# Kernel tuning notes

Measured on AMD Instinct MI355X. Metric: run time of the kernel, lower is better.

Reference implementation:

```python
import jax, jax.numpy as jnp
import numpy as np
import math

EMB_S = 64
HEADS = 8
EMB = EMB_S * HEADS  # 512
M = int(EMB_S * 0.5)  # 32 random features
B, T = 8, 4096
EPS = 1e-5


def setup_inputs() -> dict:
    key = jax.random.key(0)
    ks = jax.random.split(key, 16)
    s_in = 1.0 / math.sqrt(EMB_S)
    s_emb = 1.0 / math.sqrt(EMB)
    s_hid = 1.0 / math.sqrt(4 * EMB)
    return {
        "x": jax.random.normal(ks[0], (B, T, EMB), jnp.float32),
        "w": jax.random.normal(ks[1], (M, EMB_S), jnp.float32),  # frozen random features
        "kqv_w": jax.random.uniform(ks[2], (3 * EMB_S, EMB_S), jnp.float32, -s_in, s_in),
        "kqv_b": jax.random.uniform(ks[3], (3 * EMB_S,), jnp.float32, -s_in, s_in),
        "proj_w": jax.random.uniform(ks[4], (EMB, EMB), jnp.float32, -s_emb, s_emb),
        "proj_b": jax.random.uniform(ks[5], (EMB,), jnp.float32, -s_emb, s_emb),
        "ln1_g": 1.0 + 0.02 * jax.random.normal(ks[6], (EMB,), jnp.float32),
        "ln1_b": 0.02 * jax.random.normal(ks[7], (EMB,), jnp.float32),
        "ln2_g": 1.0 + 0.02 * jax.random.normal(ks[8], (EMB,), jnp.float32),
        "ln2_b": 0.02 * jax.random.normal(ks[9], (EMB,), jnp.float32),
        "mlp_w1": jax.random.uniform(ks[10], (4 * EMB, EMB), jnp.float32, -s_emb, s_emb),
        "mlp_b1": jax.random.uniform(ks[11], (4 * EMB,), jnp.float32, -s_emb, s_emb),
        "mlp_w2": jax.random.uniform(ks[12], (EMB, 4 * EMB), jnp.float32, -s_hid, s_hid),
        "mlp_b2": jax.random.uniform(ks[13], (EMB,), jnp.float32, -s_hid, s_hid),
    }


def _layer_norm(x, g, b):
    mu = jnp.mean(x, axis=-1, keepdims=True)
    var = jnp.mean(jnp.square(x - mu), axis=-1, keepdims=True)
    return (x - mu) * jax.lax.rsqrt(var + EPS) * g + b


def _prm_exp(z, w):
    # z: [B,T,H,E]; softmax-kernel random features, [B,T,H,M]
    xd = 0.5 * jnp.sum(z * z, axis=-1, keepdims=True)
    wtx = jnp.einsum("bthe,me->bthm", z, w)
    return jnp.exp(wtx - xd) / math.sqrt(M)


def reference(x, w, kqv_w, kqv_b, proj_w, proj_b, ln1_g, ln1_b, ln2_g, ln2_b,
              mlp_w1, mlp_b1, mlp_w2, mlp_b2):
    Bb, Tt, _ = x.shape
    h = _layer_norm(x, ln1_g, ln1_b).reshape(Bb, Tt, HEADS, EMB_S)
    kqv = jnp.einsum("bthe,fe->bthf", h, kqv_w) + kqv_b  # [B,T,H,3E]
    k, q, v = jnp.split(kqv, 3, axis=-1)  # torch.split order: k, q, v
    kp = _prm_exp(k, w)  # [B,T,H,M]
    qp = _prm_exp(q, w)
    D = jnp.einsum("bthm,bhm->bth", qp, kp.sum(axis=1))  # [B,T,H]
    kptv = jnp.einsum("bthe,bthm->bhem", v, kp)  # [B,H,E,M]
    y = jnp.einsum("bthm,bhem->bthe", qp, kptv) / D[..., None]
    y = y.reshape(Bb, Tt, EMB)
    attn = jnp.einsum("btf,ef->bte", y, proj_w) + proj_b  # dropout = identity (eval)
    x = x + attn
    h2 = _layer_norm(x, ln2_g, ln2_b)
    hid = jax.nn.gelu(jnp.einsum("bte,fe->btf", h2, mlp_w1) + mlp_b1, approximate=False)
    mlp_out = jnp.einsum("btf,ef->bte", hid, mlp_w2) + mlp_b2
    return x + mlp_out
```

## Files before the change

kernel.cpp:

```cpp
#include <hip/hip_runtime.h>
#include <hip/hip_bf16.h>

typedef __bf16 bf16x8_t __attribute__((ext_vector_type(8)));
typedef float f32x4_t __attribute__((ext_vector_type(4)));
using bf16 = __hip_bfloat16;

#define EMB 512
#define NTOK 32768
#define NROW 262144
#define SQRT_M_INV 0.17677669529663687f

__device__ __forceinline__ void gload16(const void* g, void* l) {
  __builtin_amdgcn_global_load_lds((const __attribute__((address_space(1))) void*)g,
                                   (__attribute__((address_space(3))) void*)l, 16, 0, 0);
}

__device__ __forceinline__ float fast_gelu(float v) {
  float u = v * 0.70710678118654752f;
  float a = fabsf(u);
  float tt = __builtin_amdgcn_rcpf(fmaf(0.3275911f, a, 1.0f));
  float p = fmaf(tt, 1.061405429f, -1.453152027f);
  p = fmaf(tt, p, 1.421413741f);
  p = fmaf(tt, p, -0.284496736f);
  p = fmaf(tt, p, 0.254829592f);
  p = p * tt;
  float e = __expf(-a * a);
  float er = fmaf(-p, e, 1.0f);
  er = copysignf(er, u);
  return 0.5f * v * (1.0f + er);
}

__device__ __forceinline__ void cvt4(const float* __restrict__ in,
                                     bf16* __restrict__ out, int i4, int n4) {
  if (i4 < n4) {
    float4 v = ((const float4*)in)[i4];
    alignas(8) bf16 o[4];
    o[0] = __float2bfloat16(v.x); o[1] = __float2bfloat16(v.y);
    o[2] = __float2bfloat16(v.z); o[3] = __float2bfloat16(v.w);
    *(uint2*)(out + i4 * 4) = *(const uint2*)o;
  }
}
__global__ __launch_bounds__(256) void f2b4_kernel(
    const float* __restrict__ a, bf16* __restrict__ oa, int na4,
    const float* __restrict__ b, bf16* __restrict__ ob, int nb4,
    const float* __restrict__ c, bf16* __restrict__ oc, int nc4,
    const float* __restrict__ d, bf16* __restrict__ od, int nd4) {
  int i4 = blockIdx.x * 256 + threadIdx.x;
  cvt4(a, oa, i4, na4);
  cvt4(b, ob, i4, nb4);
  cvt4(c, oc, i4, nc4);
  cvt4(d, od, i4, nd4);
}

__global__ __launch_bounds__(256) void ln_kernel(const float* __restrict__ x,
                                                 const float* __restrict__ g,
                                                 const float* __restrict__ bt,
                                                 bf16* __restrict__ out) {
  int lane = threadIdx.x & 63;
  int row = blockIdx.x * 4 + (threadIdx.x >> 6);
  const float* xr = x + (size_t)row * EMB;
  float4 v0 = ((const float4*)xr)[lane * 2];
  float4 v1 = ((const float4*)xr)[lane * 2 + 1];
  float s = v0.x + v0.y + v0.z + v0.w + v1.x + v1.y + v1.z + v1.w;
#pragma unroll
  for (int o = 32; o; o >>= 1) s += __shfl_xor(s, o);
  float mu = s * (1.0f / 512.0f);
  float vs = 0.f, d;
  d = v0.x - mu; vs += d * d;  d = v0.y - mu; vs += d * d;
  d = v0.z - mu; vs += d * d;  d = v0.w - mu; vs += d * d;
  d = v1.x - mu; vs += d * d;  d = v1.y - mu; vs += d * d;
  d = v1.z - mu; vs += d * d;  d = v1.w - mu; vs += d * d;
#pragma unroll
  for (int o = 32; o; o >>= 1) vs += __shfl_xor(vs, o);
  float rstd = rsqrtf(vs * (1.0f / 512.0f) + 1e-5f);
  float4 g0 = ((const float4*)g)[lane * 2], g1 = ((const float4*)g)[lane * 2 + 1];
  float4 b0 = ((const float4*)bt)[lane * 2], b1 = ((const float4*)bt)[lane * 2 + 1];
  alignas(16) bf16 o8[8];
  o8[0] = __float2bfloat16((v0.x - mu) * rstd * g0.x + b0.x);
  o8[1] = __float2bfloat16((v0.y - mu) * rstd * g0.y + b0.y);
  o8[2] = __float2bfloat16((v0.z - mu) * rstd * g0.z + b0.z);
  o8[3] = __float2bfloat16((v0.w - mu) * rstd * g0.w + b0.w);
  o8[4] = __float2bfloat16((v1.x - mu) * rstd * g1.x + b1.x);
  o8[5] = __float2bfloat16((v1.y - mu) * rstd * g1.y + b1.y);
  o8[6] = __float2bfloat16((v1.z - mu) * rstd * g1.z + b1.z);
  o8[7] = __float2bfloat16((v1.w - mu) * rstd * g1.w + b1.w);
  *(uint4*)(out + (size_t)row * EMB + lane * 8) = *(const uint4*)o8;
}

template <int BM, int BN, int WM, int WN, int OP>
__global__ __launch_bounds__(256) void gemm_bt(const bf16* __restrict__ A,
                                               const bf16* __restrict__ W,
                                               const float* __restrict__ bias,
                                               const float* __restrict__ res,
                                               float* __restrict__ outF,
                                               bf16* __restrict__ outB,
                                               int M, int N, int K) {
  constexpr int BK = 32;
  constexpr int TM = BM / WM, TN = BN / WN;
  constexpr int NI = TM / 16, NJ = TN / 16;
  constexpr int AP = BM * BK / 2048;
  constexpr int WP = BN * BK / 2048;
  alignas(16) __shared__ bf16 As[2][BM * BK];
  alignas(16) __shared__ bf16 Ws[2][BN * BK];
  int t = threadIdx.x;
  int lane = t & 63, wid = t >> 6;
  int wm = wid % WM, wn = wid / WM;
  int bn = blockIdx.x * BN, bm = blockIdx.y * BM;
  int lr = lane & 15, lq = lane >> 4;
  const int r0 = (t * 8) >> 5, c0 = (t * 8) & 31;

  const bf16* ap = A + (size_t)(bm + r0) * K + c0;
  const bf16* wp = W + (size_t)(bn + r0) * K + c0;
  const size_t strA = (size_t)64 * K;

  f32x4_t acc[NI][NJ];
#pragma unroll
  for (int i = 0; i < NI; ++i)
#pragma unroll
    for (int j = 0; j < NJ; ++j)
#pragma unroll
      for (int r = 0; r < 4; ++r) acc[i][j][r] = 0.f;

  auto stage = [&](int buf) {
#pragma unroll
    for (int p = 0; p < AP; ++p)
      gload16(ap + (size_t)p * strA, &As[buf][(r0 + p * 64) * BK + c0]);
#pragma unroll
    for (int p = 0; p < WP; ++p)
      gload16(wp + (size_t)p * strA, &Ws[buf][(r0 + p * 64) * BK + c0]);
    ap += BK;
    wp += BK;
  };
  auto compute = [&](int buf) {
    bf16x8_t afr[NI], bfr[NJ];
#pragma unroll
    for (int i = 0; i < NI; ++i)
      afr[i] = *(const bf16x8_t*)&As[buf][(wm * TM + i * 16 + lr) * BK + lq * 8];
#pragma unroll
    for (int j = 0; j < NJ; ++j)
      bfr[j] = *(const bf16x8_t*)&Ws[buf][(wn * TN + j * 16 + lr) * BK + lq * 8];
#pragma unroll
    for (int i = 0; i < NI; ++i)
#pragma unroll
      for (int j = 0; j < NJ; ++j)
        acc[i][j] = __builtin_amdgcn_mfma_f32_16x16x32_bf16(afr[i], bfr[j], acc[i][j], 0, 0, 0);
  };

  const int nt = K / BK;
  stage(0);
  int cur = 0;
  for (int kt = 0; kt < nt - 1; ++kt) {
    __syncthreads();
    stage(cur ^ 1);
    compute(cur);
    cur ^= 1;
  }
  __syncthreads();
  compute(cur);

#pragma unroll
  for (int i = 0; i < NI; ++i)
#pragma unroll
    for (int j = 0; j < NJ; ++j) {
      int gn = bn + wn * TN + j * 16 + lr;
      float bv = bias[gn];
#pragma unroll
      for (int r = 0; r < 4; ++r) {
        int gm = bm + wm * TM + i * 16 + lq * 4 + r;
        float v = acc[i][j][r] + bv;
        size_t off = (size_t)gm * N + gn;
        if (OP == 0) {
          outF[off] = v;
        } else if (OP == 1) {
          outF[off] = v + res[off];
        } else {
          outB[off] = __float2bfloat16(fast_gelu(v));
        }
      }
    }
}

__device__ __forceinline__ size_t bh_row(size_t grow) {
  size_t h = grow & 7, bt = grow >> 3;
  size_t b = bt >> 12, tt = bt & 4095;
  return ((b * 8 + h) << 12) + tt;
}

__global__ __launch_bounds__(256) void kqv_prm_kernel(
    const bf16* __restrict__ A,
    const bf16* __restrict__ Wk,
    const float* __restrict__ bias,
    const float* __restrict__ wrf,
    float* __restrict__ kp, float* __restrict__ qp,
    bf16* __restrict__ vout) {
  constexpr int LDZ = 136;
  constexpr int LDV = 72;
  alignas(16) __shared__ char u_raw[27648];
  bf16* As  = (bf16*)u_raw;
  bf16* Ws  = (bf16*)(u_raw + 4096);
  bf16* zkq = (bf16*)u_raw;
  bf16* vs  = (bf16*)(u_raw + 17408);
  float* xd_s = (float*)(u_raw + 26624);

  int t = threadIdx.x;
  int lane = t & 63, wid = t >> 6;
  int wm = wid & 1, wn = wid >> 1;
  int lr = lane & 15, lq = lane >> 4;
  size_t row0 = (size_t)blockIdx.x * 64;

  bf16x8_t wfrag[2][2];
#pragma unroll
  for (int mt = 0; mt < 2; ++mt)
#pragma unroll
    for (int ks = 0; ks < 2; ++ks) {
      const float* src = wrf + (mt * 16 + lr) * 64 + ks * 32 + lq * 8;
#pragma unroll
      for (int jj = 0; jj < 8; ++jj) wfrag[mt][ks][jj] = (__bf16)src[jj];
    }

  f32x4_t acc[2][6];
#pragma unroll
  for (int i = 0; i < 2; ++i)
#pragma unroll
    for (int j = 0; j < 6; ++j)
#pragma unroll
      for (int r = 0; r < 4; ++r) acc[i][j][r] = 0.f;

  const int r0 = t >> 2, c0 = (t * 8) & 31;
  for (int k0 = 0; k0 < 64; k0 += 32) {
    gload16(&A[(row0 + r0) * 64 + k0 + c0], &As[r0 * 32 + c0]);
#pragma unroll
    for (int p = 0; p < 3; ++p) {
      int r = r0 + p * 64;
      gload16(&Wk[(size_t)r * 64 + k0 + c0], &Ws[r * 32 + c0]);
    }
    __syncthreads();
    bf16x8_t af[2], bfr[6];
#pragma unroll
    for (int i = 0; i < 2; ++i)
      af[i] = *(const bf16x8_t*)&As[(wm * 32 + i * 16 + lr) * 32 + lq * 8];
#pragma unroll
    for (int j = 0; j < 6; ++j)
      bfr[j] = *(const bf16x8_t*)&Ws[(wn * 96 + j * 16 + lr) * 32 + lq * 8];
#pragma unroll
    for (int i = 0; i < 2; ++i)
#pragma unroll
      for (int j = 0; j < 6; ++j)
        acc[i][j] = __builtin_amdgcn_mfma_f32_16x16x32_bf16(af[i], bfr[j], acc[i][j], 0, 0, 0);
    __syncthreads();
  }

#pragma unroll
  for (int i = 0; i < 2; ++i)
#pragma unroll
    for (int j = 0; j < 6; ++j) {
      int col = wn * 96 + j * 16 + lr;
      float bv = bias[col];
      int rowb = wm * 32 + i * 16 + lq * 4;
#pragma unroll
      for (int r = 0; r < 4; ++r) {
        float v = acc[i][j][r] + bv;
        if (col < 128) zkq[(rowb + r) * LDZ + col] = __float2bfloat16(v);
        else           vs[(rowb + r) * LDV + (col - 128)] = __float2bfloat16(v);
      }
    }
  __syncthreads();

  if (t < 128) {
    int r = t & 63, sel = t >> 6;
    const bf16* zr = &zkq[r * LDZ + sel * 64];
    float xd = 0.f;
#pragma unroll
    for (int c = 0; c < 64; c += 8) {
      bf16x8_t z8 = *(const bf16x8_t*)&zr[c];
#pragma unroll
      for (int jj = 0; jj < 8; ++jj) { float f = (float)z8[jj]; xd += f * f; }
    }
    xd_s[r * 2 + sel] = 0.5f * xd;
  }
  __syncthreads();

#pragma unroll
  for (int p = 0; p < 2; ++p) {
    int idx = t + p * 256;
    int r = idx >> 3, c8 = idx & 7;
    size_t nr = bh_row(row0 + r);
    *(uint4*)&vout[nr * 64 + c8 * 8] = *(const uint4*)&vs[r * LDV + c8 * 8];
  }

  int sel = wn;
  f32x4_t aw[2][2];
#pragma unroll
  for (int i = 0; i < 2; ++i)
#pragma unroll
    for (int mt = 0; mt < 2; ++mt)
#pragma unroll
      for (int r = 0; r < 4; ++r) aw[i][mt][r] = 0.f;
#pragma unroll
  for (int ks = 0; ks < 2; ++ks) {
    bf16x8_t af2[2];
#pragma unroll
    for (int i = 0; i < 2; ++i)
      af2[i] = *(const bf16x8_t*)&zkq[(wm * 32 + i * 16 + lr) * LDZ + sel * 64 + ks * 32 + lq * 8];
#pragma unroll
    for (int i = 0; i < 2; ++i)
#pragma unroll
      for (int mt = 0; mt < 2; ++mt)
        aw[i][mt] = __builtin_amdgcn_mfma_f32_16x16x32_bf16(af2[i], wfrag[mt][ks], aw[i][mt], 0, 0, 0);
  }
  float* outp = sel ? qp : kp;
#pragma unroll
  for (int i = 0; i < 2; ++i)
#pragma unroll
    for (int r = 0; r < 4; ++r) {
      int row = wm * 32 + i * 16 + lq * 4 + r;
      size_t nr = bh_row(row0 + row);
#pragma unroll
      for (int mt = 0; mt < 2; ++mt) {
        int m = mt * 16 + lr;
        outp[nr * 32 + m] =
            __expf(aw[i][mt][r] - xd_s[row * 2 + sel]) * SQRT_M_INV;
      }
    }
}

__global__ __launch_bounds__(256) void kptv_kernel(const bf16* __restrict__ v2,
                                                   const float* __restrict__ kp2,
                                                   float* __restrict__ part) {
  int bh = blockIdx.x, chunk = blockIdx.y;
  int t = threadIdx.x, e = t & 63, g = t >> 6;
  const bf16* vp = v2 + ((size_t)bh * 4096 + chunk * 512) * 64 + e;
  const float* kpp = kp2 + ((size_t)bh * 4096 + chunk * 512) * 32 + g * 8;
  float acc[8] = {0.f, 0.f, 0.f, 0.f, 0.f, 0.f, 0.f, 0.f};
  float accs[8] = {0.f, 0.f, 0.f, 0.f, 0.f, 0.f, 0.f, 0.f};
#pragma unroll 8
  for (int tok = 0; tok < 512; ++tok) {
    float vv = __bfloat162float(vp[tok * 64]);
    float4 k0 = *(const float4*)(kpp + tok * 32);
    float4 k1 = *(const float4*)(kpp + tok * 32 + 4);
    acc[0] += vv * k0.x; acc[1] += vv * k0.y; acc[2] += vv * k0.z; acc[3] += vv * k0.w;
    acc[4] += vv * k1.x; acc[5] += vv * k1.y; acc[6] += vv * k1.z; acc[7] += vv * k1.w;
    accs[0] += k0.x; accs[1] += k0.y; accs[2] += k0.z; accs[3] += k0.w;
    accs[4] += k1.x; accs[5] += k1.y; accs[6] += k1.z; accs[7] += k1.w;
  }
  float* pp = part + (size_t)(bh * 8 + chunk) * 2080 + e * 32 + g * 8;
  *(float4*)pp = make_float4(acc[0], acc[1], acc[2], acc[3]);
  *(float4*)(pp + 4) = make_float4(acc[4], acc[5], acc[6], acc[7]);
  if (e == 0) {
    float* ps = part + (size_t)(bh * 8 + chunk) * 2080 + 2048 + g * 8;
    *(float4*)ps = make_float4(accs[0], accs[1], accs[2], accs[3]);
    *(float4*)(ps + 4) = make_float4(accs[4], accs[5], accs[6], accs[7]);
  }
}

__global__ __launch_bounds__(256) void y_kernel(const float* __restrict__ qp2,
                                                const float* __restrict__ part,
                                                bf16* __restrict__ y) {
  int bh = blockIdx.x, chunk = blockIdx.y;
  int b = bh >> 3, h = bh & 7;
  alignas(16) __shared__ float qp_s[16][32];
  int t = threadIdx.x;
  int e = t & 63, iq = t >> 6;
  float kv[32], ks[32];
#pragma unroll
  for (int m = 0; m < 32; ++m) { kv[m] = 0.f; ks[m] = 0.f; }
  for (int c = 0; c < 8; ++c) {
    const float* pp = part + (size_t)(bh * 8 + c) * 2080;
#pragma unroll
    for (int m = 0; m < 32; m += 4) {
      float4 a = *(const float4*)&pp[e * 32 + m];
      kv[m] += a.x; kv[m + 1] += a.y; kv[m + 2] += a.z; kv[m + 3] += a.w;
      float4 s = *(const float4*)&pp[2048 + m];
      ks[m] += s.x; ks[m + 1] += s.y; ks[m + 2] += s.z; ks[m + 3] += s.w;
    }
  }
  for (int grp = 0; grp < 32; ++grp) {
    int tok0 = chunk * 512 + grp * 16;
    __syncthreads();
    if (t < 128) {
      int r = t >> 3, c4 = t & 7;
      *(float4*)&qp_s[r][c4 * 4] =
          *(const float4*)(qp2 + ((size_t)bh * 4096 + tok0 + r) * 32 + c4 * 4);
    }
    __syncthreads();
#pragma unroll
    for (int i0 = 0; i0 < 4; ++i0) {
      int i = iq * 4 + i0;
      float dot = 0.f, dd = 0.f;
#pragma unroll
      for (int m = 0; m < 32; m += 4) {
        float4 qq = *(const float4*)&qp_s[i][m];
        dot += qq.x * kv[m] + qq.y * kv[m + 1] + qq.z * kv[m + 2] + qq.w * kv[m + 3];
        dd  += qq.x * ks[m] + qq.y * ks[m + 1] + qq.z * ks[m + 2] + qq.w * ks[m + 3];
      }
      y[(size_t)(b * 4096 + tok0 + i) * EMB + h * 64 + e] = __float2bfloat16(dot / dd);
    }
  }
}

extern "C" void kernel_launch(void* const* d_in, const int* in_sizes, int n_in,
                              void* d_out, int out_size, void* d_ws, size_t ws_size,
                              hipStream_t stream) {
  const float* x      = (const float*)d_in[0];
  const float* w      = (const float*)d_in[1];
  const float* kqv_w  = (const float*)d_in[2];
  const float* kqv_b  = (const float*)d_in[3];
  const float* proj_w = (const float*)d_in[4];
  const float* proj_b = (const float*)d_in[5];
  const float* ln1_g  = (const float*)d_in[6];
  const float* ln1_b  = (const float*)d_in[7];
  const float* ln2_g  = (const float*)d_in[8];
  const float* ln2_b  = (const float*)d_in[9];
  const float* mlp_w1 = (const float*)d_in[10];
  const float* mlp_b1 = (const float*)d_in[11];
  const float* mlp_w2 = (const float*)d_in[12];
  const float* mlp_b2 = (const float*)d_in[13];
  float* out = (float*)d_out;

  char* ws = (char*)d_ws;
  size_t off = 0;
  auto alloc = [&](size_t bytes) -> void* {
    void* p = ws + off;
    off = (off + bytes + 255) & ~(size_t)255;
    return p;
  };

  bf16* kqv_wb  = (bf16*)alloc(12288 * 2);
  bf16* proj_wb = (bf16*)alloc(262144 * 2);
  bf16* w1b     = (bf16*)alloc(1048576 * 2);
  bf16* w2b     = (bf16*)alloc(1048576 * 2);
  bf16* hb      = (bf16*)alloc((size_t)NTOK * EMB * 2);
  bf16* yb      = hb;
  float* qpb    = (float*)alloc((size_t)NROW * 32 * 4);
  bf16* h2b     = (bf16*)qpb;
  float* kpb    = (float*)alloc((size_t)NROW * 32 * 4);
  bf16* hidb    = (bf16*)kpb;
  bf16* vb      = (bf16*)alloc((size_t)NROW * 64 * 2);
  float* partb  = (float*)alloc((size_t)512 * 2080 * 4);

  f2b4_kernel<<<1024, 256, 0, stream>>>(kqv_w, kqv_wb, 12288 / 4,
                                        proj_w, proj_wb, 262144 / 4,
                                        mlp_w1, w1b, 1048576 / 4,
                                        mlp_w2, w2b, 1048576 / 4);

  ln_kernel<<<NTOK / 4, 256, 0, stream>>>(x, ln1_g, ln1_b, hb);

  kqv_prm_kernel<<<NROW / 64, 256, 0, stream>>>(hb, kqv_wb, kqv_b, w, kpb, qpb, vb);

  kptv_kernel<<<dim3(64, 8), 256, 0, stream>>>(vb, kpb, partb);

  y_kernel<<<dim3(64, 8), 256, 0, stream>>>(qpb, partb, yb);

  gemm_bt<128, 128, 2, 2, 1><<<dim3(4, NTOK / 128), 256, 0, stream>>>(
      yb, proj_wb, proj_b, x, out, nullptr, NTOK, 512, 512);

  ln_kernel<<<NTOK / 4, 256, 0, stream>>>(out, ln2_g, ln2_b, h2b);

  for (int c = 0; c < 2; ++c) {
    const bf16* h2c = h2b + (size_t)c * 16384 * 512;
    float* outc = out + (size_t)c * 16384 * 512;
    gemm_bt<128, 128, 2, 2, 2><<<dim3(16, 128), 256, 0, stream>>>(
        h2c, w1b, mlp_b1, nullptr, nullptr, hidb, 16384, 2048, 512);
    gemm_bt<128, 128, 2, 2, 1><<<dim3(4, 128), 256, 0, stream>>>(
        hidb, w2b, mlp_b2, outc, outc, nullptr, 16384, 512, 2048);
  }
}
```

Before: 641.6 us.

## Remap GEMM workgroups across XCDs, restructure kptv reduction, shrink MLP2 tile

Three separate changes. The GEMM block index is remapped so consecutive workgroups are spread across the 8 XCDs, aiming for better L2 locality. The kptv kernel now splits tokens into 16 chunks instead of 8; each thread handles 4 embedding columns over strided tokens and partial sums are reduced in shared memory, which raises parallelism and vectorises the v loads. The second MLP GEMM switches to 64x128 tiles with a 1x4 warp layout to launch more blocks, at the cost of less reuse per tile.

```diff
diff --git a/kernel.cpp b/kernel.cpp
--- a/kernel.cpp
+++ b/kernel.cpp
@@ -9,6 +9,7 @@
 #define NTOK 32768
 #define NROW 262144
 #define SQRT_M_INV 0.17677669529663687f
+#define KNC 16
 
 __device__ __forceinline__ void gload16(const void* g, void* l) {
   __builtin_amdgcn_global_load_lds((const __attribute__((address_space(1))) void*)g,
@@ -105,7 +106,10 @@
   int t = threadIdx.x;
   int lane = t & 63, wid = t >> 6;
   int wm = wid % WM, wn = wid / WM;
-  int bn = blockIdx.x * BN, bm = blockIdx.y * BM;
+  int nwg = gridDim.x * gridDim.y;
+  int lin = blockIdx.y * gridDim.x + blockIdx.x;
+  if ((nwg & 7) == 0) lin = (lin & 7) * (nwg >> 3) + (lin >> 3);
+  int bn = (lin % gridDim.x) * BN, bm = (lin / gridDim.x) * BM;
   int lr = lane & 15, lq = lane >> 4;
   const int r0 = (t * 8) >> 5, c0 = (t * 8) & 31;
 
@@ -328,28 +332,68 @@
                                                    const float* __restrict__ kp2,
                                                    float* __restrict__ part) {
   int bh = blockIdx.x, chunk = blockIdx.y;
-  int t = threadIdx.x, e = t & 63, g = t >> 6;
-  const bf16* vp = v2 + ((size_t)bh * 4096 + chunk * 512) * 64 + e;
-  const float* kpp = kp2 + ((size_t)bh * 4096 + chunk * 512) * 32 + g * 8;
-  float acc[8] = {0.f, 0.f, 0.f, 0.f, 0.f, 0.f, 0.f, 0.f};
-  float accs[8] = {0.f, 0.f, 0.f, 0.f, 0.f, 0.f, 0.f, 0.f};
-#pragma unroll 8
-  for (int tok = 0; tok < 512; ++tok) {
-    float vv = __bfloat162float(vp[tok * 64]);
-    float4 k0 = *(const float4*)(kpp + tok * 32);
-    float4 k1 = *(const float4*)(kpp + tok * 32 + 4);
-    acc[0] += vv * k0.x; acc[1] += vv * k0.y; acc[2] += vv * k0.z; acc[3] += vv * k0.w;
-    acc[4] += vv * k1.x; acc[5] += vv * k1.y; acc[6] += vv * k1.z; acc[7] += vv * k1.w;
-    accs[0] += k0.x; accs[1] += k0.y; accs[2] += k0.z; accs[3] += k0.w;
-    accs[4] += k1.x; accs[5] += k1.y; accs[6] += k1.z; accs[7] += k1.w;
-  }
-  float* pp = part + (size_t)(bh * 8 + chunk) * 2080 + e * 32 + g * 8;
-  *(float4*)pp = make_float4(acc[0], acc[1], acc[2], acc[3]);
-  *(float4*)(pp + 4) = make_float4(acc[4], acc[5], acc[6], acc[7]);
-  if (e == 0) {
-    float* ps = part + (size_t)(bh * 8 + chunk) * 2080 + 2048 + g * 8;
-    *(float4*)ps = make_float4(accs[0], accs[1], accs[2], accs[3]);
-    *(float4*)(ps + 4) = make_float4(accs[4], accs[5], accs[6], accs[7]);
+  int t = threadIdx.x;
+  int ts = t >> 6;
+  int eg = (t >> 2) & 15;
+  int g  = t & 3;
+  const int T0 = chunk * 256;
+  const bf16* vp = v2 + ((size_t)bh * 4096 + T0) * 64 + eg * 4;
+  const float* kpp = kp2 + ((size_t)bh * 4096 + T0) * 32 + g * 8;
+
+  float acc[4][8];
+  float accs[8];
+#pragma unroll
+  for (int e = 0; e < 4; ++e)
+#pragma unroll
+    for (int m = 0; m < 8; ++m) acc[e][m] = 0.f;
+#pragma unroll
+  for (int m = 0; m < 8; ++m) accs[m] = 0.f;
+
+#pragma unroll 2
+  for (int tok = ts; tok < 256; tok += 4) {
+    union { uint2 u; ushort s[4]; } vr;
+    vr.u = *(const uint2*)(vp + (size_t)tok * 64);
+    float ve[4];
+#pragma unroll
+    for (int e = 0; e < 4; ++e)
+      ve[e] = __uint_as_float((uint32_t)vr.s[e] << 16);
+    float4 k0 = *(const float4*)(kpp + (size_t)tok * 32);
+    float4 k1 = *(const float4*)(kpp + (size_t)tok * 32 + 4);
+    float km[8] = {k0.x, k0.y, k0.z, k0.w, k1.x, k1.y, k1.z, k1.w};
+#pragma unroll
+    for (int e = 0; e < 4; ++e)
+#pragma unroll
+      for (int m = 0; m < 8; ++m) acc[e][m] = fmaf(ve[e], km[m], acc[e][m]);
+#pragma unroll
+    for (int m = 0; m < 8; ++m) accs[m] += km[m];
+  }
+
+  __shared__ float red[256][33];
+  __shared__ float reds[4][4][8];
+#pragma unroll
+  for (int e = 0; e < 4; ++e)
+#pragma unroll
+    for (int m = 0; m < 8; ++m) red[t][e * 8 + m] = acc[e][m];
+  if (eg == 0) {
+#pragma unroll
+    for (int m = 0; m < 8; ++m) reds[ts][g][m] = accs[m];
+  }
+  __syncthreads();
+
+  int l = t >> 2, q = t & 3;
+  int leg = l >> 2, lg = l & 3;
+  float o[8];
+#pragma unroll
+  for (int m = 0; m < 8; ++m)
+    o[m] = red[l][q * 8 + m] + red[l + 64][q * 8 + m] +
+           red[l + 128][q * 8 + m] + red[l + 192][q * 8 + m];
+  float* pp = part + (size_t)(bh * KNC + chunk) * 2080 + (leg * 4 + q) * 32 + lg * 8;
+  *(float4*)pp = make_float4(o[0], o[1], o[2], o[3]);
+  *(float4*)(pp + 4) = make_float4(o[4], o[5], o[6], o[7]);
+  if (t < 32) {
+    int g2 = t >> 3, j = t & 7;
+    float s = reds[0][g2][j] + reds[1][g2][j] + reds[2][g2][j] + reds[3][g2][j];
+    part[(size_t)(bh * KNC + chunk) * 2080 + 2048 + g2 * 8 + j] = s;
   }
 }
 
@@ -364,8 +408,8 @@
   float kv[32], ks[32];
 #pragma unroll
   for (int m = 0; m < 32; ++m) { kv[m] = 0.f; ks[m] = 0.f; }
-  for (int c = 0; c < 8; ++c) {
-    const float* pp = part + (size_t)(bh * 8 + c) * 2080;
+  for (int c = 0; c < KNC; ++c) {
+    const float* pp = part + (size_t)(bh * KNC + c) * 2080;
 #pragma unroll
     for (int m = 0; m < 32; m += 4) {
       float4 a = *(const float4*)&pp[e * 32 + m];
@@ -436,7 +480,7 @@
   float* kpb    = (float*)alloc((size_t)NROW * 32 * 4);
   bf16* hidb    = (bf16*)kpb;
   bf16* vb      = (bf16*)alloc((size_t)NROW * 64 * 2);
-  float* partb  = (float*)alloc((size_t)512 * 2080 * 4);
+  float* partb  = (float*)alloc((size_t)64 * KNC * 2080 * 4);
 
   f2b4_kernel<<<1024, 256, 0, stream>>>(kqv_w, kqv_wb, 12288 / 4,
                                         proj_w, proj_wb, 262144 / 4,
@@ -447,7 +491,7 @@
 
   kqv_prm_kernel<<<NROW / 64, 256, 0, stream>>>(hb, kqv_wb, kqv_b, w, kpb, qpb, vb);
 
-  kptv_kernel<<<dim3(64, 8), 256, 0, stream>>>(vb, kpb, partb);
+  kptv_kernel<<<dim3(64, KNC), 256, 0, stream>>>(vb, kpb, partb);
 
   y_kernel<<<dim3(64, 8), 256, 0, stream>>>(qpb, partb, yb);
 
@@ -461,7 +505,7 @@
     float* outc = out + (size_t)c * 16384 * 512;
     gemm_bt<128, 128, 2, 2, 2><<<dim3(16, 128), 256, 0, stream>>>(
         h2c, w1b, mlp_b1, nullptr, nullptr, hidb, 16384, 2048, 512);
-    gemm_bt<128, 128, 2, 2, 1><<<dim3(4, 128), 256, 0, stream>>>(
+    gemm_bt<64, 128, 1, 4, 1><<<dim3(4, 256), 256, 0, stream>>>(
         hidb, w2b, mlp_b2, outc, outc, nullptr, 16384, 512, 2048);
   }
 }
```

After: 604.0 us. -5.9%, faster.
